# Kernel tuning notes

Hardware: AMD Instinct MI355X
Metric: run time of the kernel (lower is better)

Reference implementation:

```python
import jax, jax.numpy as jnp
import numpy as np
import math

D_MODEL = 1024
HEADS = 16
D_K = D_MODEL // HEADS
BATCH = 4
SEQ = 1024


def setup_inputs() -> dict:
    key = jax.random.key(0)
    ks = jax.random.split(key, 12)
    s = 1.0 / math.sqrt(D_MODEL)
    inp = {
        "q": jax.random.normal(ks[0], (BATCH, SEQ, D_MODEL), jnp.float32),
        "k": jax.random.normal(ks[1], (BATCH, SEQ, D_MODEL), jnp.float32),
        "v": jax.random.normal(ks[2], (BATCH, SEQ, D_MODEL), jnp.float32),
        # causal mask, broadcastable over (batch, heads)
        "mask": jnp.tril(jnp.ones((SEQ, SEQ), jnp.bool_))[None, None, :, :],
        "Wq": jax.random.normal(ks[3], (D_MODEL, D_MODEL), jnp.float32) * s,
        "bq": jax.random.normal(ks[4], (D_MODEL,), jnp.float32) * 0.01,
        "Wk": jax.random.normal(ks[5], (D_MODEL, D_MODEL), jnp.float32) * s,
        "bk": jax.random.normal(ks[6], (D_MODEL,), jnp.float32) * 0.01,
        "Wv": jax.random.normal(ks[7], (D_MODEL, D_MODEL), jnp.float32) * s,
        "bv": jax.random.normal(ks[8], (D_MODEL,), jnp.float32) * 0.01,
        "Wo": jax.random.normal(ks[9], (D_MODEL, D_MODEL), jnp.float32) * s,
        "bo": jax.random.normal(ks[10], (D_MODEL,), jnp.float32) * 0.01,
    }
    return inp


def reference(q, k, v, mask, Wq, bq, Wk, bk, Wv, bv, Wo, bo):
    B, S, _ = q.shape
    # projections (torch Linear: x @ W.T + b; here W stored as [in, out])
    def proj(x, W, b):
        return (x @ W + b).reshape(B, -1, HEADS, D_K).transpose(0, 2, 1, 3)

    Q = proj(q, Wq, bq)  # [B, H, S, Dk]
    K = proj(k, Wk, bk)
    V = proj(v, Wv, bv)

    scores = jnp.einsum("bhqd,bhkd->bhqk", Q, K) / math.sqrt(D_K)
    scores = jnp.where(mask, scores, jnp.float32(-1e9))
    attn = jax.nn.softmax(scores, axis=-1)  # dropout p=0.0 -> identity
    x = jnp.einsum("bhqk,bhkd->bhqd", attn, V)
    x = x.transpose(0, 2, 1, 3).reshape(B, S, D_MODEL)
    return x @ Wo + bo
```

## Files before the change

### kernel.cpp

```cpp
#include <hip/hip_runtime.h>
#include <math.h>

typedef __bf16 bf16_t;
typedef bf16_t bf16x8 __attribute__((ext_vector_type(8)));
typedef bf16_t bf16x4 __attribute__((ext_vector_type(4)));
typedef float  floatx4 __attribute__((ext_vector_type(4)));
typedef unsigned int u32;

#define MFMA_BF16(a, b, c) __builtin_amdgcn_mfma_f32_16x16x32_bf16((a), (b), (c), 0, 0, 0)

#if __has_builtin(__builtin_amdgcn_exp2f)
#define EXP2F(x) __builtin_amdgcn_exp2f(x)
#else
#define EXP2F(x) exp2f(x)
#endif

static constexpr int DMODEL = 1024;
static constexpr int NHEAD  = 16;
static constexpr int HDIM   = 64;
static constexpr int NBATCH = 4;
static constexpr int SEQLEN = 1024;
static constexpr int NTOK   = NBATCH * SEQLEN;

typedef __attribute__((address_space(3))) void       as3_void;
typedef __attribute__((address_space(1))) const void as1_cvoid;

__device__ __forceinline__ void gload16(const void* g, void* l) {
    __builtin_amdgcn_global_load_lds((as1_cvoid*)g, (as3_void*)l, 16, 0, 0);
}

__device__ __forceinline__ bf16x8 load_cvt8(const float* __restrict__ p) {
    floatx4 a = *(const floatx4*)p;
    floatx4 b = *(const floatx4*)(p + 4);
    bf16x8 r;
    r[0] = (bf16_t)a[0]; r[1] = (bf16_t)a[1]; r[2] = (bf16_t)a[2]; r[3] = (bf16_t)a[3];
    r[4] = (bf16_t)b[0]; r[5] = (bf16_t)b[1]; r[6] = (bf16_t)b[2]; r[7] = (bf16_t)b[3];
    return r;
}

__global__ __launch_bounds__(256) void prep(
    const float* __restrict__ W0, const float* __restrict__ W1,
    const float* __restrict__ W2, const float* __restrict__ W3,
    const float* __restrict__ q, const float* __restrict__ k, const float* __restrict__ v,
    bf16_t* __restrict__ Wt, bf16_t* __restrict__ Xr)
{
    __shared__ float tile[32][33];
    const int z = blockIdx.z;
    if (z < 4) {
        const float* W = (z == 0) ? W0 : (z == 1) ? W1 : (z == 2) ? W2 : W3;
        bf16_t* O = Wt + (size_t)z * DMODEL * DMODEL;
        const int tx = threadIdx.x & 31, ty = threadIdx.x >> 5;
        const int r0 = blockIdx.x * 32, c0 = blockIdx.y * 32;
#pragma unroll
        for (int i = 0; i < 32; i += 8)
            tile[ty + i][tx] = W[(size_t)(r0 + ty + i) * DMODEL + c0 + tx];
        __syncthreads();
#pragma unroll
        for (int i = 0; i < 32; i += 8)
            O[(size_t)(c0 + ty + i) * DMODEL + r0 + tx] = (bf16_t)tile[tx][ty + i];
    } else {
        const float* src = (z == 4) ? q : (z == 5) ? k : v;
        bf16_t* dst = Xr + (size_t)(z - 4) * ((size_t)NTOK * DMODEL);
        size_t i = (((size_t)blockIdx.y * 32 + blockIdx.x) * 256 + threadIdx.x) * 16;
        *(bf16x8*)(dst + i)     = load_cvt8(src + i);
        *(bf16x8*)(dst + i + 8) = load_cvt8(src + i + 8);
    }
}

__global__ __launch_bounds__(256) void transpose_w(
    const float* __restrict__ W0, const float* __restrict__ W1,
    const float* __restrict__ W2, const float* __restrict__ W3,
    bf16_t* __restrict__ out)
{
    __shared__ float tile[32][33];
    const float* W = (blockIdx.z == 0) ? W0 : (blockIdx.z == 1) ? W1
                   : (blockIdx.z == 2) ? W2 : W3;
    bf16_t* O = out + (size_t)blockIdx.z * DMODEL * DMODEL;
    int tx = threadIdx.x, ty = threadIdx.y;
    int r0 = blockIdx.x * 32, c0 = blockIdx.y * 32;
#pragma unroll
    for (int i = 0; i < 32; i += 8)
        tile[ty + i][tx] = W[(size_t)(r0 + ty + i) * DMODEL + c0 + tx];
    __syncthreads();
#pragma unroll
    for (int i = 0; i < 32; i += 8)
        O[(size_t)(c0 + ty + i) * DMODEL + r0 + tx] = (bf16_t)tile[tx][ty + i];
}
__global__ __launch_bounds__(256) void cvt_bf16(
    const float* __restrict__ src, bf16_t* __restrict__ dst)
{
    size_t i = ((size_t)blockIdx.x * 256 + threadIdx.x) * 8;
    *(bf16x8*)(dst + i) = load_cvt8(src + i);
}

__global__ __launch_bounds__(256) void gemm_qkv(
    const bf16_t* __restrict__ Xb, size_t astride, int mode0,
    const bf16_t* __restrict__ Wt,
    const float* __restrict__ bq, const float* __restrict__ bk, const float* __restrict__ bv,
    bf16_t* __restrict__ Qh, bf16_t* __restrict__ Kh, bf16_t* __restrict__ Vt)
{
    const int mode = mode0 + blockIdx.z;
    const bf16_t* A = Xb + astride * (size_t)blockIdx.z;
    const bf16_t* B = Wt + (size_t)mode * DMODEL * DMODEL;
    const float* bias = (mode == 0) ? bq : (mode == 1) ? bk : bv;
    bf16_t* out       = (mode == 0) ? Qh : (mode == 1) ? Kh : Vt;

    __shared__ __align__(16) bf16_t lA[2][128 * 32];
    __shared__ __align__(16) bf16_t lB[2][128 * 32];

    const int wave = threadIdx.x >> 6, lane = threadIdx.x & 63;
    const int quad = lane >> 4, l15 = lane & 15;
    const int wm = wave >> 1, wn = wave & 1;
    const int row0 = blockIdx.x * 128, col0 = blockIdx.y * 128;
    const int srow = lane >> 2, scol = (lane & 3) * 8;

    const floatx4 zero = {0.f, 0.f, 0.f, 0.f};
    floatx4 acc[4][4];
#pragma unroll
    for (int mt = 0; mt < 4; mt++)
#pragma unroll
        for (int nt = 0; nt < 4; nt++) acc[mt][nt] = zero;

#pragma unroll
    for (int j = 0; j < 2; j++) {
        const int seg = j * 4 + wave;
        gload16(A + (size_t)(row0 + seg * 16 + srow) * DMODEL + scol, lA[0] + seg * 512);
        gload16(B + (size_t)(col0 + seg * 16 + srow) * DMODEL + scol, lB[0] + seg * 512);
    }

    for (int it = 0; it < 32; it++) {
        __syncthreads();
        const int cur = it & 1;
        if (it + 1 < 32) {
            const int k1 = (it + 1) * 32;
            const int nb = cur ^ 1;
#pragma unroll
            for (int j = 0; j < 2; j++) {
                const int seg = j * 4 + wave;
                gload16(A + (size_t)(row0 + seg * 16 + srow) * DMODEL + k1 + scol, lA[nb] + seg * 512);
                gload16(B + (size_t)(col0 + seg * 16 + srow) * DMODEL + k1 + scol, lB[nb] + seg * 512);
            }
        }
        bf16x8 aF[4], bF[4];
#pragma unroll
        for (int t = 0; t < 4; t++) {
            aF[t] = *(const bf16x8*)(lA[cur] + (wm * 64 + t * 16 + l15) * 32 + quad * 8);
            bF[t] = *(const bf16x8*)(lB[cur] + (wn * 64 + t * 16 + l15) * 32 + quad * 8);
        }
#pragma unroll
        for (int mt = 0; mt < 4; mt++)
#pragma unroll
            for (int nt = 0; nt < 4; nt++)
                acc[mt][nt] = MFMA_BF16(aF[mt], bF[nt], acc[mt][nt]);
    }

#pragma unroll
    for (int nt = 0; nt < 4; nt++) {
        const int gn = col0 + wn * 64 + nt * 16 + l15;
        const float bb = bias[gn];
        const int hh = gn >> 6, dd = gn & 63;
#pragma unroll
        for (int mt = 0; mt < 4; mt++) {
#pragma unroll
            for (int r = 0; r < 4; r++) {
                const int tok = row0 + wm * 64 + mt * 16 + quad * 4 + r;
                const int b = tok >> 10, s = tok & 1023;
                float vv = acc[mt][nt][r] + bb;
                size_t addr;
                if (mode == 2) {
                    addr = ((size_t)((b * NHEAD + hh) * HDIM + dd)) * SEQLEN + s;
                } else {
                    if (mode == 0) vv *= 0.1803368801111204f;
                    addr = ((size_t)((b * NHEAD + hh) * SEQLEN + s)) * HDIM + dd;
                }
                out[addr] = (bf16_t)vv;
            }
        }
    }
}

__global__ __launch_bounds__(256) void gemm_o(
    const bf16_t* __restrict__ Xa, const bf16_t* __restrict__ Wt,
    const float* __restrict__ bias, float* __restrict__ out)
{
    __shared__ __align__(16) bf16_t lA[2][64 * 32];
    __shared__ __align__(16) bf16_t lB[2][128 * 32];

    const int wave = threadIdx.x >> 6, lane = threadIdx.x & 63;
    const int quad = lane >> 4, l15 = lane & 15;
    const int wm = wave & 1, wn = wave >> 1;
    const int row0 = blockIdx.x * 64, col0 = blockIdx.y * 128;
    const int srow = lane >> 2, scol = (lane & 3) * 8;

    const floatx4 zero = {0.f, 0.f, 0.f, 0.f};
    floatx4 acc[2][4];
#pragma unroll
    for (int mt = 0; mt < 2; mt++)
#pragma unroll
        for (int nt = 0; nt < 4; nt++) acc[mt][nt] = zero;

    gload16(Xa + (size_t)(row0 + wave * 16 + srow) * DMODEL + scol, lA[0] + wave * 512);
#pragma unroll
    for (int j = 0; j < 2; j++) {
        const int seg = wave * 2 + j;
        gload16(Wt + (size_t)(col0 + seg * 16 + srow) * DMODEL + scol, lB[0] + seg * 512);
    }

    for (int it = 0; it < 32; it++) {
        __syncthreads();
        const int cur = it & 1;
        if (it + 1 < 32) {
            const int k1 = (it + 1) * 32;
            const int nb = cur ^ 1;
            gload16(Xa + (size_t)(row0 + wave * 16 + srow) * DMODEL + k1 + scol, lA[nb] + wave * 512);
#pragma unroll
            for (int j = 0; j < 2; j++) {
                const int seg = wave * 2 + j;
                gload16(Wt + (size_t)(col0 + seg * 16 + srow) * DMODEL + k1 + scol, lB[nb] + seg * 512);
            }
        }
        bf16x8 aF[2], bF[4];
#pragma unroll
        for (int t = 0; t < 2; t++)
            aF[t] = *(const bf16x8*)(lA[cur] + (wm * 32 + t * 16 + l15) * 32 + quad * 8);
#pragma unroll
        for (int t = 0; t < 4; t++)
            bF[t] = *(const bf16x8*)(lB[cur] + (wn * 64 + t * 16 + l15) * 32 + quad * 8);
#pragma unroll
        for (int mt = 0; mt < 2; mt++)
#pragma unroll
            for (int nt = 0; nt < 4; nt++)
                acc[mt][nt] = MFMA_BF16(aF[mt], bF[nt], acc[mt][nt]);
    }

#pragma unroll
    for (int nt = 0; nt < 4; nt++) {
        const int gn = col0 + wn * 64 + nt * 16 + l15;
        const float bb = bias[gn];
#pragma unroll
        for (int mt = 0; mt < 2; mt++) {
#pragma unroll
            for (int r = 0; r < 4; r++) {
                const int tok = row0 + wm * 32 + mt * 16 + quad * 4 + r;
                out[(size_t)tok * DMODEL + gn] = acc[mt][nt][r] + bb;
            }
        }
    }
}

#define SHUF_PV(pk, Vv, oacc) do {                                                     \
    u32 a0 = __shfl(pk.u[0], srcA), a1 = __shfl(pk.u[1], srcA);                        \
    u32 a2 = __shfl(pk.u[0], srcB), a3 = __shfl(pk.u[1], srcB);                        \
    u32 b0 = __shfl(pk.u[2], srcA), b1 = __shfl(pk.u[3], srcA);                        \
    u32 b2 = __shfl(pk.u[2], srcB), b3 = __shfl(pk.u[3], srcB);                        \
    union { u32 u[4]; bf16x8 v; } bP;                                                  \
    bP.u[0] = hiP ? b0 : a0; bP.u[1] = hiP ? b1 : a1;                                  \
    bP.u[2] = hiP ? b2 : a2; bP.u[3] = hiP ? b3 : a3;                                  \
    __builtin_amdgcn_s_setprio(1);                                                     \
    _Pragma("unroll") for (int dt = 0; dt < 4; dt++)                                   \
        oacc[dt] = MFMA_BF16(Vv[dt], bP.v, oacc[dt]);                                  \
    __builtin_amdgcn_s_setprio(0);                                                     \
} while (0)

#define SOFTMAX_PV_FAST(S0x, S1x, Vv, lacc, oacc) do {                                 \
    float ps = 0.f;                                                                    \
    union { bf16_t hh2[8]; u32 u[4]; } pk;                                             \
    _Pragma("unroll") for (int r = 0; r < 4; r++) {                                    \
        float e0 = EXP2F(S0x[r]), e1 = EXP2F(S1x[r]);                                  \
        ps += e0 + e1;                                                                 \
        pk.hh2[r] = (bf16_t)e0; pk.hh2[4 + r] = (bf16_t)e1;                            \
    }                                                                                  \
    lacc += ps;                                                                        \
    SHUF_PV(pk, Vv, oacc);                                                             \
} while (0)

#define SOFTMAX_PV_MASK(S0x, S1x, Vv, kbv, qrow, lacc, oacc) do {                      \
    float ps = 0.f;                                                                    \
    union { bf16_t hh2[8]; u32 u[4]; } pk;                                             \
    _Pragma("unroll") for (int r = 0; r < 4; r++) {                                    \
        const int key0 = (kbv) + quad * 4 + r;                                         \
        float s0 = (key0 <= (qrow))      ? S0x[r] : -1e30f;                            \
        float s1 = (key0 + 16 <= (qrow)) ? S1x[r] : -1e30f;                            \
        float e0 = EXP2F(s0), e1 = EXP2F(s1);                                          \
        ps += e0 + e1;                                                                 \
        pk.hh2[r] = (bf16_t)e0; pk.hh2[4 + r] = (bf16_t)e1;                            \
    }                                                                                  \
    lacc += ps;                                                                        \
    SHUF_PV(pk, Vv, oacc);                                                             \
} while (0)

#define LOAD_KV(K0v, K1v, Vv, kbv) do {                                                \
    _Pragma("unroll") for (int c = 0; c < 2; c++) {                                    \
        K0v[c] = *(const bf16x8*)(Kp + (size_t)((kbv) + l15) * HDIM + c * 32 + quad * 8);      \
        K1v[c] = *(const bf16x8*)(Kp + (size_t)((kbv) + 16 + l15) * HDIM + c * 32 + quad * 8); \
    }                                                                                  \
    _Pragma("unroll") for (int dt = 0; dt < 4; dt++)                                   \
        Vv[dt] = *(const bf16x8*)(Vp + (size_t)(dt * 16 + l15) * SEQLEN + (kbv) + quad * 8);   \
} while (0)

#define COMPUTE(K0v, K1v, Vv, kcv) do {                                                \
    const int kb_ = (kcv) * 32;                                                        \
    const bool doA_ = (kcv) < nkA;                                                     \
    floatx4 S0B = zero, S1B = zero, S0A = zero, S1A = zero;                            \
    __builtin_amdgcn_s_setprio(1);                                                     \
    _Pragma("unroll") for (int c = 0; c < 2; c++) {                                    \
        S0B = MFMA_BF16(K0v[c], bQB[c], S0B);                                          \
        S1B = MFMA_BF16(K1v[c], bQB[c], S1B);                                          \
    }                                                                                  \
    __builtin_amdgcn_s_setprio(0);                                                     \
    if (doA_) {                                                                        \
        __builtin_amdgcn_s_setprio(1);                                                 \
        _Pragma("unroll") for (int c = 0; c < 2; c++) {                                \
            S0A = MFMA_BF16(K0v[c], bQA[c], S0A);                                      \
            S1A = MFMA_BF16(K1v[c], bQA[c], S1A);                                      \
        }                                                                              \
        __builtin_amdgcn_s_setprio(0);                                                 \
    }                                                                                  \
    if (kb_ + 31 <= qbaseB) { SOFTMAX_PV_FAST(S0B, S1B, Vv, lB_, oB); }                \
    else                    { SOFTMAX_PV_MASK(S0B, S1B, Vv, kb_, qrowB, lB_, oB); }    \
    if (doA_) {                                                                        \
        if (kb_ + 31 <= qbaseA) { SOFTMAX_PV_FAST(S0A, S1A, Vv, lA_, oA); }            \
        else                    { SOFTMAX_PV_MASK(S0A, S1A, Vv, kb_, qrowA, lA_, oA); }\
    }                                                                                  \
} while (0)

__global__ __launch_bounds__(256, 2) void attn(
    const bf16_t* __restrict__ Qh, const bf16_t* __restrict__ Kh,
    const bf16_t* __restrict__ Vt, bf16_t* __restrict__ X)
{
    __shared__ __align__(8) float comb[2][64][34];
    const int wave = threadIdx.x >> 6, lane = threadIdx.x & 63;
    const int quad = lane >> 4, l15 = lane & 15;
    const int L = blockIdx.x;
    const int bh = (L & 7) * 8 + ((L >> 3) & 7);
    const int t  = L >> 6;
    const int b = bh >> 4, h = bh & 15;

    const int qbaseA = 16 * t, qbaseB = 1008 - 16 * t;
    const int qrowA = qbaseA + l15, qrowB = qbaseB + l15;
    const int nkA = t / 2 + 1, nkB = 32 - t / 2;

    const bf16_t* Qp = Qh + (size_t)bh * SEQLEN * HDIM;
    const bf16_t* Kp = Kh + (size_t)bh * SEQLEN * HDIM;
    const bf16_t* Vp = Vt + (size_t)bh * HDIM * SEQLEN;

    bf16x8 bQA[2], bQB[2];
#pragma unroll
    for (int c = 0; c < 2; c++) {
        bQA[c] = *(const bf16x8*)(Qp + (size_t)qrowA * HDIM + c * 32 + quad * 8);
        bQB[c] = *(const bf16x8*)(Qp + (size_t)qrowB * HDIM + c * 32 + quad * 8);
    }

    const floatx4 zero = {0.f, 0.f, 0.f, 0.f};
    float lA_ = 0.f, lB_ = 0.f;
    floatx4 oA[4], oB[4];
#pragma unroll
    for (int dt = 0; dt < 4; dt++) { oA[dt] = zero; oB[dt] = zero; }

    const int srcA = ((quad & 1) ? 32 : 0) + l15;
    const int srcB = srcA + 16;
    const bool hiP = (quad >= 2);

    bf16x8 K0x[2], K1x[2], Vx[4];
    bf16x8 K0y[2], K1y[2], Vy[4];
    int kc = wave;
    LOAD_KV(K0x, K1x, Vx, kc * 32);
    __builtin_amdgcn_sched_barrier(0);
    for (; kc + 4 < nkB; kc += 8) {
        LOAD_KV(K0y, K1y, Vy, (kc + 4) * 32);
        __builtin_amdgcn_sched_barrier(0);
        COMPUTE(K0x, K1x, Vx, kc);
        if (kc + 8 < nkB) {
            LOAD_KV(K0x, K1x, Vx, (kc + 8) * 32);
            __builtin_amdgcn_sched_barrier(0);
        }
        COMPUTE(K0y, K1y, Vy, kc + 4);
    }
    if (kc < nkB) COMPUTE(K0x, K1x, Vx, kc);

    auto publish = [&](int slot) {
        float2* d2 = (float2*)&comb[slot][lane][0];
#pragma unroll
        for (int dt = 0; dt < 4; dt++) {
            d2[2 * dt]     = make_float2(oA[dt][0], oA[dt][1]);
            d2[2 * dt + 1] = make_float2(oA[dt][2], oA[dt][3]);
            d2[8 + 2 * dt]     = make_float2(oB[dt][0], oB[dt][1]);
            d2[8 + 2 * dt + 1] = make_float2(oB[dt][2], oB[dt][3]);
        }
        d2[16] = make_float2(lA_, lB_);
    };
    auto accum = [&](int slot) {
        const float2* s2 = (const float2*)&comb[slot][lane][0];
#pragma unroll
        for (int dt = 0; dt < 4; dt++) {
            float2 x0 = s2[2 * dt], x1 = s2[2 * dt + 1];
            float2 y0 = s2[8 + 2 * dt], y1 = s2[8 + 2 * dt + 1];
            oA[dt][0] += x0.x; oA[dt][1] += x0.y; oA[dt][2] += x1.x; oA[dt][3] += x1.y;
            oB[dt][0] += y0.x; oB[dt][1] += y0.y; oB[dt][2] += y1.x; oB[dt][3] += y1.y;
        }
        float2 lp = s2[16];
        lA_ += lp.x; lB_ += lp.y;
    };

    if (wave & 1) publish(wave >> 1);
    __syncthreads();
    if (!(wave & 1)) accum(wave >> 1);
    __syncthreads();
    if (wave == 2) publish(0);
    __syncthreads();
    if (wave == 0) {
        accum(0);

        lA_ += __shfl_xor(lA_, 16); lA_ += __shfl_xor(lA_, 32);
        lB_ += __shfl_xor(lB_, 16); lB_ += __shfl_xor(lB_, 32);

        const float invA = 1.f / lA_, invB = 1.f / lB_;
#pragma unroll
        for (int dt = 0; dt < 4; dt++) {
            bf16x4 va, vb;
#pragma unroll
            for (int r = 0; r < 4; r++) {
                va[r] = (bf16_t)(oA[dt][r] * invA);
                vb[r] = (bf16_t)(oB[dt][r] * invB);
            }
            const size_t cofs = (size_t)h * HDIM + dt * 16 + quad * 4;
            *(bf16x4*)(&X[((size_t)(b * SEQLEN + qrowA)) * DMODEL + cofs]) = va;
            *(bf16x4*)(&X[((size_t)(b * SEQLEN + qrowB)) * DMODEL + cofs]) = vb;
        }
    }
}

extern "C" void kernel_launch(void* const* d_in, const int* in_sizes, int n_in,
                              void* d_out, int out_size, void* d_ws, size_t ws_size,
                              hipStream_t stream)
{
    const float* q  = (const float*)d_in[0];
    const float* k  = (const float*)d_in[1];
    const float* v  = (const float*)d_in[2];
    const float* Wq = (const float*)d_in[4];
    const float* bq = (const float*)d_in[5];
    const float* Wk = (const float*)d_in[6];
    const float* bk = (const float*)d_in[7];
    const float* Wv = (const float*)d_in[8];
    const float* bv = (const float*)d_in[9];
    const float* Wo = (const float*)d_in[10];
    const float* bo = (const float*)d_in[11];
    float* out = (float*)d_out;

    char* ws = (char*)d_ws;
    const size_t MB = 1ull << 20;
    const size_t NELEM = (size_t)NTOK * DMODEL;
    bf16_t* Wt = (bf16_t*)ws;
    bf16_t* Qh = (bf16_t*)(ws + 8 * MB);
    bf16_t* Kh = (bf16_t*)(ws + 16 * MB);
    bf16_t* Vt = (bf16_t*)(ws + 24 * MB);
    bf16_t* Xr = (bf16_t*)(ws + 32 * MB);

    if (ws_size >= 56 * MB) {
        prep<<<dim3(32, 32, 7), dim3(256), 0, stream>>>(Wq, Wk, Wv, Wo, q, k, v, Wt, Xr);
        gemm_qkv<<<dim3(32, 8, 3), dim3(256), 0, stream>>>(
            Xr, NELEM, 0, Wt, bq, bk, bv, Qh, Kh, Vt);
    } else {
        transpose_w<<<dim3(32, 32, 4), dim3(32, 8), 0, stream>>>(Wq, Wk, Wv, Wo, Wt);
        const float* qkv_in[3] = {q, k, v};
        for (int m = 0; m < 3; m++) {
            cvt_bf16<<<dim3(2048), dim3(256), 0, stream>>>(qkv_in[m], Xr);
            gemm_qkv<<<dim3(32, 8, 1), dim3(256), 0, stream>>>(
                Xr, 0, m, Wt, bq, bk, bv, Qh, Kh, Vt);
        }
    }

    bf16_t* Xa = Xr;
    attn<<<dim3(2048), dim3(256), 0, stream>>>(Qh, Kh, Vt, Xa);
    gemm_o<<<dim3(64, 8), dim3(256), 0, stream>>>(
        Xa, Wt + 3 * (size_t)DMODEL * DMODEL, bo, out);
}
```

Baseline: 237.4 us.

## Process four query tiles per attention block to reuse K/V loads

Each attention block now handles four 16-row query tiles (two low, two high causal tiles) instead of two, so the grid is halved and every K/V chunk loaded from global memory serves twice as many query rows. The manual double-buffered K/V prefetch loop is replaced with a simpler one-chunk-per-iteration loop, and the shared combine buffer is doubled to hold four accumulators. The change cuts redundant K/V traffic but raises register pressure, which under the launch bounds risks spills or lower occupancy. Dropping the explicit prefetch may also expose load latency.

```diff
diff --git a/kernel.cpp b/kernel.cpp
--- a/kernel.cpp
+++ b/kernel.cpp
@@ -298,108 +298,118 @@
         Vv[dt] = *(const bf16x8*)(Vp + (size_t)(dt * 16 + l15) * SEQLEN + (kbv) + quad * 8);   \
 } while (0)
 
-#define COMPUTE(K0v, K1v, Vv, kcv) do {                                                \
-    const int kb_ = (kcv) * 32;                                                        \
-    const bool doA_ = (kcv) < nkA;                                                     \
-    floatx4 S0B = zero, S1B = zero, S0A = zero, S1A = zero;                            \
-    __builtin_amdgcn_s_setprio(1);                                                     \
-    _Pragma("unroll") for (int c = 0; c < 2; c++) {                                    \
-        S0B = MFMA_BF16(K0v[c], bQB[c], S0B);                                          \
-        S1B = MFMA_BF16(K1v[c], bQB[c], S1B);                                          \
-    }                                                                                  \
-    __builtin_amdgcn_s_setprio(0);                                                     \
-    if (doA_) {                                                                        \
-        __builtin_amdgcn_s_setprio(1);                                                 \
-        _Pragma("unroll") for (int c = 0; c < 2; c++) {                                \
-            S0A = MFMA_BF16(K0v[c], bQA[c], S0A);                                      \
-            S1A = MFMA_BF16(K1v[c], bQA[c], S1A);                                      \
-        }                                                                              \
-        __builtin_amdgcn_s_setprio(0);                                                 \
-    }                                                                                  \
-    if (kb_ + 31 <= qbaseB) { SOFTMAX_PV_FAST(S0B, S1B, Vv, lB_, oB); }                \
-    else                    { SOFTMAX_PV_MASK(S0B, S1B, Vv, kb_, qrowB, lB_, oB); }    \
-    if (doA_) {                                                                        \
-        if (kb_ + 31 <= qbaseA) { SOFTMAX_PV_FAST(S0A, S1A, Vv, lA_, oA); }            \
-        else                    { SOFTMAX_PV_MASK(S0A, S1A, Vv, kb_, qrowA, lA_, oA); }\
-    }                                                                                  \
-} while (0)
-
 __global__ __launch_bounds__(256, 2) void attn(
     const bf16_t* __restrict__ Qh, const bf16_t* __restrict__ Kh,
     const bf16_t* __restrict__ Vt, bf16_t* __restrict__ X)
 {
-    __shared__ __align__(8) float comb[2][64][34];
+    __shared__ __align__(8) float comb[2][64][68];
     const int wave = threadIdx.x >> 6, lane = threadIdx.x & 63;
     const int quad = lane >> 4, l15 = lane & 15;
     const int L = blockIdx.x;
     const int bh = (L & 7) * 8 + ((L >> 3) & 7);
-    const int t  = L >> 6;
+    const int j  = L >> 6;
     const int b = bh >> 4, h = bh & 15;
 
-    const int qbaseA = 16 * t, qbaseB = 1008 - 16 * t;
-    const int qrowA = qbaseA + l15, qrowB = qbaseB + l15;
-    const int nkA = t / 2 + 1, nkB = 32 - t / 2;
+    const int qbase0 = 32 * j,        qbase1 = 32 * j + 16;
+    const int qbase2 = 992 - 32 * j,  qbase3 = 1008 - 32 * j;
+    const int qrow0 = qbase0 + l15, qrow1 = qbase1 + l15;
+    const int qrow2 = qbase2 + l15, qrow3 = qbase3 + l15;
+    const int NKA = j + 1, NKB = 32 - j;
 
     const bf16_t* Qp = Qh + (size_t)bh * SEQLEN * HDIM;
     const bf16_t* Kp = Kh + (size_t)bh * SEQLEN * HDIM;
     const bf16_t* Vp = Vt + (size_t)bh * HDIM * SEQLEN;
 
-    bf16x8 bQA[2], bQB[2];
+    bf16x8 bQ0[2], bQ1[2], bQ2[2], bQ3[2];
 #pragma unroll
     for (int c = 0; c < 2; c++) {
-        bQA[c] = *(const bf16x8*)(Qp + (size_t)qrowA * HDIM + c * 32 + quad * 8);
-        bQB[c] = *(const bf16x8*)(Qp + (size_t)qrowB * HDIM + c * 32 + quad * 8);
+        bQ0[c] = *(const bf16x8*)(Qp + (size_t)qrow0 * HDIM + c * 32 + quad * 8);
+        bQ1[c] = *(const bf16x8*)(Qp + (size_t)qrow1 * HDIM + c * 32 + quad * 8);
+        bQ2[c] = *(const bf16x8*)(Qp + (size_t)qrow2 * HDIM + c * 32 + quad * 8);
+        bQ3[c] = *(const bf16x8*)(Qp + (size_t)qrow3 * HDIM + c * 32 + quad * 8);
     }
 
     const floatx4 zero = {0.f, 0.f, 0.f, 0.f};
-    float lA_ = 0.f, lB_ = 0.f;
-    floatx4 oA[4], oB[4];
-#pragma unroll
-    for (int dt = 0; dt < 4; dt++) { oA[dt] = zero; oB[dt] = zero; }
+    float l0_ = 0.f, l1_ = 0.f, l2_ = 0.f, l3_ = 0.f;
+    floatx4 o0[4], o1[4], o2[4], o3[4];
+#pragma unroll
+    for (int dt = 0; dt < 4; dt++) { o0[dt] = zero; o1[dt] = zero; o2[dt] = zero; o3[dt] = zero; }
 
     const int srcA = ((quad & 1) ? 32 : 0) + l15;
     const int srcB = srcA + 16;
     const bool hiP = (quad >= 2);
 
-    bf16x8 K0x[2], K1x[2], Vx[4];
-    bf16x8 K0y[2], K1y[2], Vy[4];
-    int kc = wave;
-    LOAD_KV(K0x, K1x, Vx, kc * 32);
-    __builtin_amdgcn_sched_barrier(0);
-    for (; kc + 4 < nkB; kc += 8) {
-        LOAD_KV(K0y, K1y, Vy, (kc + 4) * 32);
-        __builtin_amdgcn_sched_barrier(0);
-        COMPUTE(K0x, K1x, Vx, kc);
-        if (kc + 8 < nkB) {
-            LOAD_KV(K0x, K1x, Vx, (kc + 8) * 32);
-            __builtin_amdgcn_sched_barrier(0);
-        }
-        COMPUTE(K0y, K1y, Vy, kc + 4);
-    }
-    if (kc < nkB) COMPUTE(K0x, K1x, Vx, kc);
+    for (int kc = wave; kc < NKB; kc += 4) {
+        const int kb = kc * 32;
+        bf16x8 K0[2], K1[2], Vv[4];
+        LOAD_KV(K0, K1, Vv, kb);
+
+        const bool doA = (kc < NKA);
+        floatx4 S0_0 = zero, S1_0 = zero, S0_1 = zero, S1_1 = zero;
+        floatx4 S0_2 = zero, S1_2 = zero, S0_3 = zero, S1_3 = zero;
+        __builtin_amdgcn_s_setprio(1);
+#pragma unroll
+        for (int c = 0; c < 2; c++) {
+            S0_2 = MFMA_BF16(K0[c], bQ2[c], S0_2);
+            S1_2 = MFMA_BF16(K1[c], bQ2[c], S1_2);
+            S0_3 = MFMA_BF16(K0[c], bQ3[c], S0_3);
+            S1_3 = MFMA_BF16(K1[c], bQ3[c], S1_3);
+        }
+        __builtin_amdgcn_s_setprio(0);
+        if (doA) {
+            __builtin_amdgcn_s_setprio(1);
+#pragma unroll
+            for (int c = 0; c < 2; c++) {
+                S0_0 = MFMA_BF16(K0[c], bQ0[c], S0_0);
+                S1_0 = MFMA_BF16(K1[c], bQ0[c], S1_0);
+                S0_1 = MFMA_BF16(K0[c], bQ1[c], S0_1);
+                S1_1 = MFMA_BF16(K1[c], bQ1[c], S1_1);
+            }
+            __builtin_amdgcn_s_setprio(0);
+        }
+        if (kb + 31 <= qbase2) { SOFTMAX_PV_FAST(S0_2, S1_2, Vv, l2_, o2); }
+        else                   { SOFTMAX_PV_MASK(S0_2, S1_2, Vv, kb, qrow2, l2_, o2); }
+        if (kb + 31 <= qbase3) { SOFTMAX_PV_FAST(S0_3, S1_3, Vv, l3_, o3); }
+        else                   { SOFTMAX_PV_MASK(S0_3, S1_3, Vv, kb, qrow3, l3_, o3); }
+        if (doA) {
+            if (kb + 31 <= qbase0) { SOFTMAX_PV_FAST(S0_0, S1_0, Vv, l0_, o0); }
+            else                   { SOFTMAX_PV_MASK(S0_0, S1_0, Vv, kb, qrow0, l0_, o0); }
+            if (kb + 31 <= qbase1) { SOFTMAX_PV_FAST(S0_1, S1_1, Vv, l1_, o1); }
+            else                   { SOFTMAX_PV_MASK(S0_1, S1_1, Vv, kb, qrow1, l1_, o1); }
+        }
+    }
 
     auto publish = [&](int slot) {
         float2* d2 = (float2*)&comb[slot][lane][0];
 #pragma unroll
         for (int dt = 0; dt < 4; dt++) {
-            d2[2 * dt]     = make_float2(oA[dt][0], oA[dt][1]);
-            d2[2 * dt + 1] = make_float2(oA[dt][2], oA[dt][3]);
-            d2[8 + 2 * dt]     = make_float2(oB[dt][0], oB[dt][1]);
-            d2[8 + 2 * dt + 1] = make_float2(oB[dt][2], oB[dt][3]);
-        }
-        d2[16] = make_float2(lA_, lB_);
+            d2[ 0 + 2 * dt]     = make_float2(o0[dt][0], o0[dt][1]);
+            d2[ 0 + 2 * dt + 1] = make_float2(o0[dt][2], o0[dt][3]);
+            d2[ 8 + 2 * dt]     = make_float2(o1[dt][0], o1[dt][1]);
+            d2[ 8 + 2 * dt + 1] = make_float2(o1[dt][2], o1[dt][3]);
+            d2[16 + 2 * dt]     = make_float2(o2[dt][0], o2[dt][1]);
+            d2[16 + 2 * dt + 1] = make_float2(o2[dt][2], o2[dt][3]);
+            d2[24 + 2 * dt]     = make_float2(o3[dt][0], o3[dt][1]);
+            d2[24 + 2 * dt + 1] = make_float2(o3[dt][2], o3[dt][3]);
+        }
+        d2[32] = make_float2(l0_, l1_);
+        d2[33] = make_float2(l2_, l3_);
     };
     auto accum = [&](int slot) {
         const float2* s2 = (const float2*)&comb[slot][lane][0];
 #pragma unroll
         for (int dt = 0; dt < 4; dt++) {
-            float2 x0 = s2[2 * dt], x1 = s2[2 * dt + 1];
-            float2 y0 = s2[8 + 2 * dt], y1 = s2[8 + 2 * dt + 1];
-            oA[dt][0] += x0.x; oA[dt][1] += x0.y; oA[dt][2] += x1.x; oA[dt][3] += x1.y;
-            oB[dt][0] += y0.x; oB[dt][1] += y0.y; oB[dt][2] += y1.x; oB[dt][3] += y1.y;
-        }
-        float2 lp = s2[16];
-        lA_ += lp.x; lB_ += lp.y;
+            float2 p0 = s2[ 0 + 2 * dt], p1 = s2[ 0 + 2 * dt + 1];
+            float2 q0 = s2[ 8 + 2 * dt], q1 = s2[ 8 + 2 * dt + 1];
+            float2 r0 = s2[16 + 2 * dt], r1 = s2[16 + 2 * dt + 1];
+            float2 t0 = s2[24 + 2 * dt], t1 = s2[24 + 2 * dt + 1];
+            o0[dt][0] += p0.x; o0[dt][1] += p0.y; o0[dt][2] += p1.x; o0[dt][3] += p1.y;
+            o1[dt][0] += q0.x; o1[dt][1] += q0.y; o1[dt][2] += q1.x; o1[dt][3] += q1.y;
+            o2[dt][0] += r0.x; o2[dt][1] += r0.y; o2[dt][2] += r1.x; o2[dt][3] += r1.y;
+            o3[dt][0] += t0.x; o3[dt][1] += t0.y; o3[dt][2] += t1.x; o3[dt][3] += t1.y;
+        }
+        float2 la = s2[32], lb = s2[33];
+        l0_ += la.x; l1_ += la.y; l2_ += lb.x; l3_ += lb.y;
     };
 
     if (wave & 1) publish(wave >> 1);
@@ -411,21 +421,27 @@
     if (wave == 0) {
         accum(0);
 
-        lA_ += __shfl_xor(lA_, 16); lA_ += __shfl_xor(lA_, 32);
-        lB_ += __shfl_xor(lB_, 16); lB_ += __shfl_xor(lB_, 32);
-
-        const float invA = 1.f / lA_, invB = 1.f / lB_;
+        l0_ += __shfl_xor(l0_, 16); l0_ += __shfl_xor(l0_, 32);
+        l1_ += __shfl_xor(l1_, 16); l1_ += __shfl_xor(l1_, 32);
+        l2_ += __shfl_xor(l2_, 16); l2_ += __shfl_xor(l2_, 32);
+        l3_ += __shfl_xor(l3_, 16); l3_ += __shfl_xor(l3_, 32);
+
+        const float i0 = 1.f / l0_, i1 = 1.f / l1_, i2 = 1.f / l2_, i3 = 1.f / l3_;
 #pragma unroll
         for (int dt = 0; dt < 4; dt++) {
-            bf16x4 va, vb;
+            bf16x4 v0, v1, v2, v3;
 #pragma unroll
             for (int r = 0; r < 4; r++) {
-                va[r] = (bf16_t)(oA[dt][r] * invA);
-                vb[r] = (bf16_t)(oB[dt][r] * invB);
+                v0[r] = (bf16_t)(o0[dt][r] * i0);
+                v1[r] = (bf16_t)(o1[dt][r] * i1);
+                v2[r] = (bf16_t)(o2[dt][r] * i2);
+                v3[r] = (bf16_t)(o3[dt][r] * i3);
             }
             const size_t cofs = (size_t)h * HDIM + dt * 16 + quad * 4;
-            *(bf16x4*)(&X[((size_t)(b * SEQLEN + qrowA)) * DMODEL + cofs]) = va;
-            *(bf16x4*)(&X[((size_t)(b * SEQLEN + qrowB)) * DMODEL + cofs]) = vb;
+            *(bf16x4*)(&X[((size_t)(b * SEQLEN + qrow0)) * DMODEL + cofs]) = v0;
+            *(bf16x4*)(&X[((size_t)(b * SEQLEN + qrow1)) * DMODEL + cofs]) = v1;
+            *(bf16x4*)(&X[((size_t)(b * SEQLEN + qrow2)) * DMODEL + cofs]) = v2;
+            *(bf16x4*)(&X[((size_t)(b * SEQLEN + qrow3)) * DMODEL + cofs]) = v3;
         }
     }
 }
@@ -471,7 +487,7 @@
     }
 
     bf16_t* Xa = Xr;
-    attn<<<dim3(2048), dim3(256), 0, stream>>>(Qh, Kh, Vt, Xa);
+    attn<<<dim3(1024), dim3(256), 0, stream>>>(Qh, Kh, Vt, Xa);
     gemm_o<<<dim3(64, 8), dim3(256), 0, stream>>>(
         Xa, Wt + 3 * (size_t)DMODEL * DMODEL, bo, out);
 }
```

New measurement: 219.9 us. 7.4% less time.
